# Optimization experiments

Hardware: AMD Instinct MI355X
Metric: run time of the kernel (lower is better)

Reference implementation:

```python
import jax, jax.numpy as jnp
import numpy as np

B, S, D, H = 2, 2048, 512, 8
HD = D // H  # head_size = 64
EPS = 1e-5


def _layer_norm(x, g, b):
    m = jnp.mean(x, axis=-1, keepdims=True)
    v = jnp.mean(jnp.square(x - m), axis=-1, keepdims=True)
    return (x - m) * jax.lax.rsqrt(v + EPS) * g + b


def setup_inputs() -> dict:
    key = jax.random.key(0)
    ks = jax.random.split(key, 16)
    s_in = 1.0 / np.sqrt(D)
    s_ff = 1.0 / np.sqrt(4 * D)
    return {
        "x": jax.random.normal(ks[0], (B, S, D), jnp.float32),
        # per-head q/k/v projections stacked over heads: [H, D, HD]
        "Wq": jax.random.normal(ks[1], (H, D, HD), jnp.float32) * s_in,
        "bq": jax.random.normal(ks[2], (H, HD), jnp.float32) * s_in,
        "Wk": jax.random.normal(ks[3], (H, D, HD), jnp.float32) * s_in,
        "bk": jax.random.normal(ks[4], (H, HD), jnp.float32) * s_in,
        "Wv": jax.random.normal(ks[5], (H, D, HD), jnp.float32) * s_in,
        "bv": jax.random.normal(ks[6], (H, HD), jnp.float32) * s_in,
        "Wp": jax.random.normal(ks[7], (D, D), jnp.float32) * s_in,
        "bp": jax.random.normal(ks[8], (D,), jnp.float32) * s_in,
        "W1": jax.random.normal(ks[9], (D, 4 * D), jnp.float32) * s_in,
        "b1": jax.random.normal(ks[10], (4 * D,), jnp.float32) * s_in,
        "W2": jax.random.normal(ks[11], (4 * D, D), jnp.float32) * s_ff,
        "b2": jax.random.normal(ks[12], (D,), jnp.float32) * s_ff,
        "g1": jnp.ones((D,), jnp.float32),
        "be1": jnp.zeros((D,), jnp.float32),
        "g2": jnp.ones((D,), jnp.float32),
        "be2": jnp.zeros((D,), jnp.float32),
    }


def reference(x, Wq, bq, Wk, bk, Wv, bv, Wp, bp, W1, b1, W2, b2, g1, be1, g2, be2):
    # --- attention sublayer (pre-norm) ---
    xn = _layer_norm(x, g1, be1)                               # [B,S,D]
    q = jnp.einsum('bsd,hde->bhse', xn, Wq) + bq[None, :, None, :]
    k = jnp.einsum('bsd,hde->bhse', xn, Wk) + bk[None, :, None, :]
    v = jnp.einsum('bsd,hde->bhse', xn, Wv) + bv[None, :, None, :]
    # NOTE: original has NO 1/sqrt(head_size) scaling and NO mask
    scores = jnp.einsum('bhse,bhte->bhst', q, k)               # [B,H,S,S]
    w = jax.nn.softmax(scores, axis=-1)
    o = jnp.einsum('bhst,bhte->bhse', w, v)                    # [B,H,S,HD]
    o = o.transpose(0, 2, 1, 3).reshape(x.shape[0], x.shape[1], D)  # concat heads
    attn_out = o @ Wp + bp
    x = x + attn_out
    # --- MLP sublayer (pre-norm) ---
    xn2 = _layer_norm(x, g2, be2)
    h = jax.nn.relu(xn2 @ W1 + b1)
    x = x + (h @ W2 + b2)
    return x
```

## Files before the change

### kernel.cpp

```cpp
#include <hip/hip_runtime.h>
#include <hip/hip_bf16.h>

typedef unsigned short u16;
typedef unsigned long long u64t;
typedef __attribute__((ext_vector_type(8))) short bhalf8;
typedef __attribute__((ext_vector_type(4))) short bhalf4;
typedef __attribute__((ext_vector_type(4))) float f32x4;

#define MFMA16(a, b, c) __builtin_amdgcn_mfma_f32_16x16x32_bf16((a), (b), (c), 0, 0, 0)

#if __has_builtin(__builtin_amdgcn_mfma_f32_16x16x16bf16_1k)
#define HAVE_K16 1
#define MFMAK16(a, b, c) __builtin_amdgcn_mfma_f32_16x16x16bf16_1k((a), (b), (c), 0, 0, 0)
#elif __has_builtin(__builtin_amdgcn_mfma_f32_16x16x16_bf16)
#define HAVE_K16 1
#define MFMAK16(a, b, c) __builtin_amdgcn_mfma_f32_16x16x16_bf16((a), (b), (c), 0, 0, 0)
#else
#define HAVE_K16 0
#endif

#define BB 2
#define SS 2048
#define DD 512
#define HH 8
#define HD 64
#define NT (BB * SS)
#define LOG2E 1.44269504f

#if __has_builtin(__builtin_amdgcn_exp2f)
#define EXP2(x) __builtin_amdgcn_exp2f(x)
#else
#define EXP2(x) exp2f(x)
#endif

__device__ __forceinline__ u16 f2b(float f) {
    unsigned u = __builtin_bit_cast(unsigned, f);
    unsigned r = (u + 0x7fffu + ((u >> 16) & 1u)) >> 16;
    return (u16)r;
}

__device__ __forceinline__ void gl2lds16(const u16* g, u16* l) {
    u16* gn = (u16*)g;
    __builtin_amdgcn_global_load_lds((__attribute__((address_space(1))) void*)gn,
                                     (__attribute__((address_space(3))) void*)l, 16, 0, 0);
}

__global__ __launch_bounds__(256) void k_prep(const float* __restrict__ Wq, const float* __restrict__ Wk,
                                              const float* __restrict__ Wv, const float* __restrict__ Wp,
                                              const float* __restrict__ W1, const float* __restrict__ W2,
                                              const float* __restrict__ bq, const float* __restrict__ bk,
                                              const float* __restrict__ bv,
                                              u16* __restrict__ WqkvT, u16* __restrict__ WpT,
                                              u16* __restrict__ W1T, u16* __restrict__ W2T,
                                              float* __restrict__ biasqkv) {
    int j = blockIdx.x;
    int tx = threadIdx.x, ty = threadIdx.y;
    if (j >= 3072) {
        int i = (j - 3072) * 256 + ty * 32 + tx;
        biasqkv[i] = (i < 512) ? bq[i] : (i < 1024) ? bk[i - 512] : bv[i - 1024];
        return;
    }
    __shared__ float tile[32][33];
    const float* src; u16* dst; int R, C, tr, tc;
    if (j < 768) {
        int m = j >> 8, rem = j & 255, h = rem >> 5, tl = rem & 31;
        tr = tl >> 1; tc = tl & 1;
        src = (m == 0 ? Wq : (m == 1 ? Wk : Wv)) + h * 32768;
        dst = WqkvT + m * 262144 + h * 32768;
        R = 512; C = 64;
    } else if (j < 1024) { int tl = j - 768;  tr = tl >> 4; tc = tl & 15; src = Wp; dst = WpT; R = 512;  C = 512;  }
    else if (j < 2048)   { int tl = j - 1024; tr = tl >> 6; tc = tl & 63; src = W1; dst = W1T; R = 512;  C = 2048; }
    else                 { int tl = j - 2048; tr = tl >> 4; tc = tl & 15; src = W2; dst = W2T; R = 2048; C = 512;  }
    int c = tc * 32 + tx;
#pragma unroll
    for (int i = 0; i < 4; i++)
        tile[ty + i * 8][tx] = src[(size_t)(tr * 32 + ty + i * 8) * C + c];
    __syncthreads();
    int r2 = tr * 32 + tx;
#pragma unroll
    for (int i = 0; i < 4; i++)
        dst[(size_t)(tc * 32 + ty + i * 8) * R + r2] = f2b(tile[tx][ty + i * 8]);
}

__global__ __launch_bounds__(256) void k_layernorm(const float* __restrict__ x,
                                                   const float* __restrict__ g,
                                                   const float* __restrict__ be,
                                                   u16* __restrict__ out) {
    int wave = threadIdx.x >> 6, lane = threadIdx.x & 63;
    int row = blockIdx.x * 4 + wave;
    const float* xr = x + (size_t)row * DD;
    int c = lane * 8;
    float4 v0 = *(const float4*)(xr + c);
    float4 v1 = *(const float4*)(xr + c + 4);
    float s  = v0.x + v0.y + v0.z + v0.w + v1.x + v1.y + v1.z + v1.w;
    float sq = v0.x*v0.x + v0.y*v0.y + v0.z*v0.z + v0.w*v0.w
             + v1.x*v1.x + v1.y*v1.y + v1.z*v1.z + v1.w*v1.w;
#pragma unroll
    for (int m = 1; m < 64; m <<= 1) {
        s  += __shfl_xor(s, m);
        sq += __shfl_xor(sq, m);
    }
    float mean = s * (1.0f / DD);
    float var  = sq * (1.0f / DD) - mean * mean;
    float rstd = rsqrtf(var + 1e-5f);
    float4 g0 = *(const float4*)(g + c);
    float4 g1 = *(const float4*)(g + c + 4);
    float4 b0 = *(const float4*)(be + c);
    float4 b1 = *(const float4*)(be + c + 4);
    float xv[8] = {v0.x, v0.y, v0.z, v0.w, v1.x, v1.y, v1.z, v1.w};
    float gv[8] = {g0.x, g0.y, g0.z, g0.w, g1.x, g1.y, g1.z, g1.w};
    float bv[8] = {b0.x, b0.y, b0.z, b0.w, b1.x, b1.y, b1.z, b1.w};
    union { bhalf8 v; u16 u[8]; } pk;
#pragma unroll
    for (int i = 0; i < 8; i++) pk.u[i] = f2b((xv[i] - mean) * rstd * gv[i] + bv[i]);
    *(bhalf8*)(out + (size_t)row * DD + c) = pk.v;
}

template<int BM, int BN, int WR, int WC, int MI, int NI, int MODE>
__global__ __launch_bounds__(256) void k_gemm(const u16* __restrict__ A, const u16* __restrict__ Bt,
                                              const float* __restrict__ bias,
                                              int lda, int ldb, int kLen, int N,
                                              const float* __restrict__ resid,
                                              float* __restrict__ outF, u16* __restrict__ outB,
                                              u16* __restrict__ qd, u16* __restrict__ kd,
                                              u16* __restrict__ vtd) {
    constexpr int WM = MI * 16;
    constexpr int WN = NI * 16;
    static_assert(WR * WM == BM && WC * WN == BN && WR * WC == 4, "cfg");
    constexpr int ACH = BM / 32;
    constexpr int BCH = BN / 32;
    __shared__ u16 As[BM * 64];
    __shared__ u16 Bs[BN * 64];
    int t = threadIdx.x;
    int wave = t >> 6, lane = t & 63, quad = lane >> 4, l16 = lane & 15;
    int wr, wc;
    if (WC == 1)      { wr = wave; wc = 0; }
    else if (WR == 1) { wr = 0;    wc = wave; }
    else              { wr = wave >> 1; wc = wave & 1; }
    int m0 = blockIdx.y * BM, n0 = blockIdx.x * BN;

    f32x4 acc[MI][NI] = {};

    int srow = lane >> 3;
    int scol = (lane & 7) * 8;
    const u16* Ag = A  + (size_t)(m0 + srow) * lda + scol;
    const u16* Bg = Bt + (size_t)(n0 + srow) * ldb + scol;

    for (int k0 = 0; k0 < kLen; k0 += 64) {
        __syncthreads();
#pragma unroll
        for (int c = 0; c < ACH; c++) {
            int ch = wave * ACH + c;
            gl2lds16(Ag + (size_t)(ch * 8) * lda + k0, &As[ch * 512]);
        }
#pragma unroll
        for (int c = 0; c < BCH; c++) {
            int ch = wave * BCH + c;
            gl2lds16(Bg + (size_t)(ch * 8) * ldb + k0, &Bs[ch * 512]);
        }
        __syncthreads();
#pragma unroll
        for (int h = 0; h < 2; h++) {
            bhalf8 af[MI], bf[NI];
#pragma unroll
            for (int mi = 0; mi < MI; mi++)
                af[mi] = *(bhalf8*)&As[(wr * WM + mi * 16 + l16) * 64 + h * 32 + quad * 8];
#pragma unroll
            for (int ni = 0; ni < NI; ni++)
                bf[ni] = *(bhalf8*)&Bs[(wc * WN + ni * 16 + l16) * 64 + h * 32 + quad * 8];
#pragma unroll
            for (int mi = 0; mi < MI; mi++)
#pragma unroll
                for (int ni = 0; ni < NI; ni++)
                    acc[mi][ni] = MFMA16(af[mi], bf[ni], acc[mi][ni]);
        }
    }

#pragma unroll
    for (int mi = 0; mi < MI; mi++)
#pragma unroll
        for (int ni = 0; ni < NI; ni++) {
            f32x4 a = acc[mi][ni];
            int gc = n0 + wc * WN + ni * 16 + l16;
            int gr0 = m0 + wr * WM + mi * 16 + quad * 4;
            float bsv = bias[gc];
            if (MODE == 0) {
                int mm = gc >> 9, cc = gc & 511;
                int hh = cc >> 6, e = cc & 63;
                int b = gr0 >> 11, s0 = gr0 & 2047;
                if (mm == 2) {
                    u64t pk = 0;
#pragma unroll
                    for (int r = 0; r < 4; r++) pk |= (u64t)f2b(a[r] + bsv) << (16 * r);
                    *(u64t*)&vtd[((size_t)(b * HH + hh) * HD + e) * SS + s0] = pk;
                } else if (mm == 0) {
#pragma unroll
                    for (int r = 0; r < 4; r++)
                        qd[((size_t)(b * HH + hh) * SS + s0 + r) * HD + e] = f2b((a[r] + bsv) * LOG2E);
                } else {
#pragma unroll
                    for (int r = 0; r < 4; r++)
                        kd[((size_t)(b * HH + hh) * SS + s0 + r) * HD + e] = f2b(a[r] + bsv);
                }
            } else if (MODE == 1) {
#pragma unroll
                for (int r = 0; r < 4; r++) {
                    size_t idx = (size_t)(gr0 + r) * N + gc;
                    outF[idx] = a[r] + bsv + resid[idx];
                }
            } else {
#pragma unroll
                for (int r = 0; r < 4; r++)
                    outB[(size_t)(gr0 + r) * N + gc] = f2b(fmaxf(a[r] + bsv, 0.0f));
            }
        }
}

__global__ __launch_bounds__(256) void k_attention(const u16* __restrict__ q,
                                                   const u16* __restrict__ k,
                                                   const u16* __restrict__ vt,
                                                   float* __restrict__ Opart,
                                                   float* __restrict__ lsum) {
    __shared__ u16 Ks[128 * 72];
    __shared__ u16 Vs[64 * 136];
    int bh = blockIdx.x, qt = blockIdx.y, kspl = blockIdx.z;
    int t = threadIdx.x, wave = t >> 6, lane = t & 63, quad = lane >> 4, l16 = lane & 15;
    const u16* qb = q  + (size_t)bh * SS * HD;
    const u16* kb = k  + (size_t)bh * SS * HD;
    const u16* vb = vt + (size_t)bh * HD * SS;

    int srow = qt * 64 + wave * 16 + l16;
    bhalf8 qf0 = *(const bhalf8*)(qb + (size_t)srow * HD + quad * 8);
    bhalf8 qf1 = *(const bhalf8*)(qb + (size_t)srow * HD + 32 + quad * 8);

    f32x4 oacc[4] = {};
    float rsum = 0.f;

    int kr = t >> 1, kc = (t & 1) * 32;
    int vr = t >> 2, vc = (t & 3) * 32;
    const u16* kp = kb + ((size_t)kspl * 1024 + kr) * HD + kc;
    const u16* vp = vb + (size_t)vr * SS + kspl * 1024 + vc;
    u16* ksd = &Ks[kr * 72 + kc];
    u16* vsd = &Vs[vr * 136 + vc];

    bhalf8 kreg[4], vreg[4];
#pragma unroll
    for (int i = 0; i < 4; i++) {
        kreg[i] = *(const bhalf8*)(kp + i * 8);
        vreg[i] = *(const bhalf8*)(vp + i * 8);
    }

    for (int it = 0; it < 8; it++) {
        __syncthreads();
#pragma unroll
        for (int i = 0; i < 4; i++) {
            *(bhalf8*)(ksd + i * 8) = kreg[i];
            *(bhalf8*)(vsd + i * 8) = vreg[i];
        }
        __syncthreads();
        if (it < 7) {
            const u16* kn = kp + (size_t)(it + 1) * 128 * HD;
            const u16* vn = vp + (it + 1) * 128;
#pragma unroll
            for (int i = 0; i < 4; i++) {
                kreg[i] = *(const bhalf8*)(kn + i * 8);
                vreg[i] = *(const bhalf8*)(vn + i * 8);
            }
        }

        f32x4 sacc[8];
#pragma unroll
        for (int nt = 0; nt < 8; nt++) {
            bhalf8 kf0 = *(bhalf8*)&Ks[(nt * 16 + l16) * 72 + quad * 8];
            bhalf8 kf1 = *(bhalf8*)&Ks[(nt * 16 + l16) * 72 + 32 + quad * 8];
            f32x4 s = {};
            s = MFMA16(kf0, qf0, s);
            s = MFMA16(kf1, qf1, s);
            sacc[nt] = s;
        }

#if HAVE_K16
        bhalf4 pa[8];
#pragma unroll
        for (int nt = 0; nt < 8; nt++) {
            union { bhalf4 v; u16 u[4]; } pk;
#pragma unroll
            for (int r = 0; r < 4; r++) {
                float p = EXP2(sacc[nt][r]);
                rsum += p;
                pk.u[r] = f2b(p);
            }
            pa[nt] = pk.v;
        }
#pragma unroll
        for (int nt = 0; nt < 8; nt++)
#pragma unroll
            for (int et = 0; et < 4; et++) {
                bhalf4 vf = *(bhalf4*)&Vs[(et * 16 + l16) * 136 + nt * 16 + quad * 4];
                oacc[et] = MFMAK16(pa[nt], vf, oacc[et]);
            }
#else
        bhalf8 pa[8];
#pragma unroll
        for (int nt = 0; nt < 8; nt++) {
            union { bhalf8 v; u16 u[8]; } pk;
#pragma unroll
            for (int r = 0; r < 4; r++) {
                float p = EXP2(sacc[nt][r]);
                rsum += p;
                pk.u[r] = f2b(p);
            }
#pragma unroll
            for (int r = 4; r < 8; r++) pk.u[r] = 0;
            pa[nt] = pk.v;
        }
#pragma unroll
        for (int nt = 0; nt < 8; nt++)
#pragma unroll
            for (int et = 0; et < 4; et++) {
                union { bhalf8 v; bhalf4 h[2]; } vf;
                vf.h[0] = *(bhalf4*)&Vs[(et * 16 + l16) * 136 + nt * 16 + quad * 4];
                vf.h[1] = (bhalf4){0, 0, 0, 0};
                oacc[et] = MFMA16(pa[nt], vf.v, oacc[et]);
            }
#endif
    }

    rsum += __shfl_xor(rsum, 16);
    rsum += __shfl_xor(rsum, 32);

    int sbase = qt * 64 + wave * 16;
    float* Ob = Opart + ((size_t)(kspl * 16 + bh) * SS + sbase) * HD;
#pragma unroll
    for (int et = 0; et < 4; et++)
#pragma unroll
        for (int r = 0; r < 4; r++)
            Ob[(quad * 4 + r) * HD + et * 16 + l16] = oacc[et][r];
    if (quad == 0)
        lsum[(size_t)(kspl * 16 + bh) * SS + sbase + l16] = rsum;
}

__global__ __launch_bounds__(256) void k_combine(const float* __restrict__ Opart,
                                                 const float* __restrict__ lsum,
                                                 u16* __restrict__ oc) {
    int tid = blockIdx.x * 256 + threadIdx.x;
    int c4 = tid & 15, s = (tid >> 4) & 2047, bh = tid >> 15;
    size_t i0 = ((size_t)bh * SS + s) * HD + c4 * 4;
    float4 p0 = *(const float4*)(Opart + i0);
    float4 p1 = *(const float4*)(Opart + (size_t)16 * SS * HD + i0);
    float l = lsum[(size_t)bh * SS + s] + lsum[(size_t)16 * SS + (size_t)bh * SS + s];
    float inv = 1.0f / l;
    u64t pk = 0;
    pk |= (u64t)f2b((p0.x + p1.x) * inv);
    pk |= (u64t)f2b((p0.y + p1.y) * inv) << 16;
    pk |= (u64t)f2b((p0.z + p1.z) * inv) << 32;
    pk |= (u64t)f2b((p0.w + p1.w) * inv) << 48;
    int b = bh >> 3, h = bh & 7;
    *(u64t*)&oc[((size_t)b * SS + s) * DD + h * HD + c4 * 4] = pk;
}

extern "C" void kernel_launch(void* const* d_in, const int* in_sizes, int n_in,
                              void* d_out, int out_size, void* d_ws, size_t ws_size,
                              hipStream_t stream) {
    const float* x   = (const float*)d_in[0];
    const float* Wq  = (const float*)d_in[1];
    const float* bq  = (const float*)d_in[2];
    const float* Wk  = (const float*)d_in[3];
    const float* bk  = (const float*)d_in[4];
    const float* Wv  = (const float*)d_in[5];
    const float* bv  = (const float*)d_in[6];
    const float* Wp  = (const float*)d_in[7];
    const float* bp  = (const float*)d_in[8];
    const float* W1  = (const float*)d_in[9];
    const float* b1  = (const float*)d_in[10];
    const float* W2  = (const float*)d_in[11];
    const float* b2  = (const float*)d_in[12];
    const float* g1  = (const float*)d_in[13];
    const float* be1 = (const float*)d_in[14];
    const float* g2  = (const float*)d_in[15];
    const float* be2 = (const float*)d_in[16];

    char* ws = (char*)d_ws;
    u16*   WqkvT   = (u16*)(ws + 0);
    u16*   WpT     = (u16*)(ws + 1572864);
    u16*   W1T     = (u16*)(ws + 2097152);
    u16*   W2T     = (u16*)(ws + 4194304);
    float* biasqkv = (float*)(ws + 6291456);
    u16*   xn      = (u16*)(ws + 6297600);
    u16*   qB      = (u16*)(ws + 10491904);
    u16*   kB      = (u16*)(ws + 14686208);
    u16*   vTb     = (u16*)(ws + 18880512);
    u16*   oc      = (u16*)(ws + 23074816);
    float* x1      = (float*)(ws + 27269120);
    u16*   xn2     = (u16*)(ws + 35657728);
    u16*   hbuf    = (u16*)(ws + 39852032);
    float* Opart   = (float*)hbuf;
    float* lsum    = (float*)xn;

    k_prep<<<3078, dim3(32, 8), 0, stream>>>(Wq, Wk, Wv, Wp, W1, W2, bq, bk, bv,
                                             WqkvT, WpT, W1T, W2T, biasqkv);
    k_layernorm<<<NT / 4, 256, 0, stream>>>(x, g1, be1, xn);
    k_gemm<64, 128, 1, 4, 4, 2, 0><<<dim3(12, 64), 256, 0, stream>>>(
        xn, WqkvT, biasqkv, 512, 512, 512, 1536, nullptr, nullptr, nullptr, qB, kB, vTb);
    k_attention<<<dim3(16, 32, 2), 256, 0, stream>>>(qB, kB, vTb, Opart, lsum);
    k_combine<<<2048, 256, 0, stream>>>(Opart, lsum, oc);
    k_gemm<64, 64, 2, 2, 2, 2, 1><<<dim3(8, 64), 256, 0, stream>>>(
        oc, WpT, bp, 512, 512, 512, 512, x, x1, nullptr, nullptr, nullptr, nullptr);
    k_layernorm<<<NT / 4, 256, 0, stream>>>(x1, g2, be2, xn2);
    k_gemm<64, 128, 1, 4, 4, 2, 2><<<dim3(16, 64), 256, 0, stream>>>(
        xn2, W1T, b1, 512, 512, 512, 2048, nullptr, nullptr, hbuf, nullptr, nullptr, nullptr);
    k_gemm<64, 64, 2, 2, 2, 2, 1><<<dim3(8, 64), 256, 0, stream>>>(
        hbuf, W2T, b2, 2048, 2048, 2048, 512, x1, (float*)d_out, nullptr, nullptr, nullptr, nullptr);
}
```

Before: 213.2 us.

## Deepen GEMM K-tile to 128, use fixed 2x2 warp grid, double attention query rows per wave

The GEMM kernel now stages 128-wide K slices in LDS instead of 64, halving the number of barrier-separated load/compute iterations. It also switches to a fixed 2x2 wave layout for all configurations. The attention kernel processes 32 query rows per wave (two 16-row groups), so each K/V tile loaded into LDS is reused across twice as many queries, halving the grid in the query dimension. The softmax/PV stage is fused per key sub-tile to limit register pressure, but extra accumulators and the larger LDS footprint may reduce occupancy.

```diff
diff --git a/kernel.cpp b/kernel.cpp
--- a/kernel.cpp
+++ b/kernel.cpp
@@ -116,7 +116,7 @@
     *(bhalf8*)(out + (size_t)row * DD + c) = pk.v;
 }
 
-template<int BM, int BN, int WR, int WC, int MI, int NI, int MODE>
+template<int BM, int BN, int MI, int NI, int MODE>
 __global__ __launch_bounds__(256) void k_gemm(const u16* __restrict__ A, const u16* __restrict__ Bt,
                                               const float* __restrict__ bias,
                                               int lda, int ldb, int kLen, int N,
@@ -126,48 +126,45 @@
                                               u16* __restrict__ vtd) {
     constexpr int WM = MI * 16;
     constexpr int WN = NI * 16;
-    static_assert(WR * WM == BM && WC * WN == BN && WR * WC == 4, "cfg");
-    constexpr int ACH = BM / 32;
-    constexpr int BCH = BN / 32;
-    __shared__ u16 As[BM * 64];
-    __shared__ u16 Bs[BN * 64];
+    static_assert(2 * WM == BM && 2 * WN == BN, "cfg");
+    constexpr int ACH = BM / 4;
+    constexpr int BCH = BN / 4;
+    __shared__ u16 As[BM * 128];
+    __shared__ u16 Bs[BN * 128];
     int t = threadIdx.x;
     int wave = t >> 6, lane = t & 63, quad = lane >> 4, l16 = lane & 15;
-    int wr, wc;
-    if (WC == 1)      { wr = wave; wc = 0; }
-    else if (WR == 1) { wr = 0;    wc = wave; }
-    else              { wr = wave >> 1; wc = wave & 1; }
+    int wr = wave >> 1, wc = wave & 1;
     int m0 = blockIdx.y * BM, n0 = blockIdx.x * BN;
 
     f32x4 acc[MI][NI] = {};
 
-    int srow = lane >> 3;
-    int scol = (lane & 7) * 8;
+    int srow = lane >> 4;
+    int scol = (lane & 15) * 8;
     const u16* Ag = A  + (size_t)(m0 + srow) * lda + scol;
     const u16* Bg = Bt + (size_t)(n0 + srow) * ldb + scol;
 
-    for (int k0 = 0; k0 < kLen; k0 += 64) {
+    for (int k0 = 0; k0 < kLen; k0 += 128) {
         __syncthreads();
 #pragma unroll
-        for (int c = 0; c < ACH; c++) {
-            int ch = wave * ACH + c;
-            gl2lds16(Ag + (size_t)(ch * 8) * lda + k0, &As[ch * 512]);
-        }
-#pragma unroll
-        for (int c = 0; c < BCH; c++) {
-            int ch = wave * BCH + c;
-            gl2lds16(Bg + (size_t)(ch * 8) * ldb + k0, &Bs[ch * 512]);
+        for (int c = 0; c < ACH / 4; c++) {
+            int ch = wave * (ACH / 4) + c;
+            gl2lds16(Ag + (size_t)(ch * 4) * lda + k0, &As[ch * 512]);
+        }
+#pragma unroll
+        for (int c = 0; c < BCH / 4; c++) {
+            int ch = wave * (BCH / 4) + c;
+            gl2lds16(Bg + (size_t)(ch * 4) * ldb + k0, &Bs[ch * 512]);
         }
         __syncthreads();
 #pragma unroll
-        for (int h = 0; h < 2; h++) {
+        for (int h = 0; h < 4; h++) {
             bhalf8 af[MI], bf[NI];
 #pragma unroll
             for (int mi = 0; mi < MI; mi++)
-                af[mi] = *(bhalf8*)&As[(wr * WM + mi * 16 + l16) * 64 + h * 32 + quad * 8];
+                af[mi] = *(bhalf8*)&As[(wr * WM + mi * 16 + l16) * 128 + h * 32 + quad * 8];
 #pragma unroll
             for (int ni = 0; ni < NI; ni++)
-                bf[ni] = *(bhalf8*)&Bs[(wc * WN + ni * 16 + l16) * 64 + h * 32 + quad * 8];
+                bf[ni] = *(bhalf8*)&Bs[(wc * WN + ni * 16 + l16) * 128 + h * 32 + quad * 8];
 #pragma unroll
             for (int mi = 0; mi < MI; mi++)
 #pragma unroll
@@ -229,12 +226,17 @@
     const u16* kb = k  + (size_t)bh * SS * HD;
     const u16* vb = vt + (size_t)bh * HD * SS;
 
-    int srow = qt * 64 + wave * 16 + l16;
-    bhalf8 qf0 = *(const bhalf8*)(qb + (size_t)srow * HD + quad * 8);
-    bhalf8 qf1 = *(const bhalf8*)(qb + (size_t)srow * HD + 32 + quad * 8);
-
-    f32x4 oacc[4] = {};
-    float rsum = 0.f;
+    bhalf8 qfa0, qfa1, qfb0, qfb1;
+    {
+        int r0 = qt * 128 + wave * 32 + l16;
+        qfa0 = *(const bhalf8*)(qb + (size_t)r0 * HD + quad * 8);
+        qfa1 = *(const bhalf8*)(qb + (size_t)r0 * HD + 32 + quad * 8);
+        qfb0 = *(const bhalf8*)(qb + (size_t)(r0 + 16) * HD + quad * 8);
+        qfb1 = *(const bhalf8*)(qb + (size_t)(r0 + 16) * HD + 32 + quad * 8);
+    }
+
+    f32x4 oacc[2][4] = {};
+    float rsa = 0.f, rsb = 0.f;
 
     int kr = t >> 1, kc = (t & 1) * 32;
     int vr = t >> 2, vc = (t & 3) * 32;
@@ -268,76 +270,68 @@
             }
         }
 
-        f32x4 sacc[8];
 #pragma unroll
         for (int nt = 0; nt < 8; nt++) {
             bhalf8 kf0 = *(bhalf8*)&Ks[(nt * 16 + l16) * 72 + quad * 8];
             bhalf8 kf1 = *(bhalf8*)&Ks[(nt * 16 + l16) * 72 + 32 + quad * 8];
-            f32x4 s = {};
-            s = MFMA16(kf0, qf0, s);
-            s = MFMA16(kf1, qf1, s);
-            sacc[nt] = s;
-        }
-
+            f32x4 sa = {}, sb = {};
+            sa = MFMA16(kf0, qfa0, sa);
+            sa = MFMA16(kf1, qfa1, sa);
+            sb = MFMA16(kf0, qfb0, sb);
+            sb = MFMA16(kf1, qfb1, sb);
 #if HAVE_K16
-        bhalf4 pa[8];
-#pragma unroll
-        for (int nt = 0; nt < 8; nt++) {
-            union { bhalf4 v; u16 u[4]; } pk;
+            union { bhalf4 v; u16 u[4]; } pa, pb;
 #pragma unroll
             for (int r = 0; r < 4; r++) {
-                float p = EXP2(sacc[nt][r]);
-                rsum += p;
-                pk.u[r] = f2b(p);
-            }
-            pa[nt] = pk.v;
-        }
-#pragma unroll
-        for (int nt = 0; nt < 8; nt++)
+                float p0 = EXP2(sa[r]);
+                float p1 = EXP2(sb[r]);
+                rsa += p0; rsb += p1;
+                pa.u[r] = f2b(p0); pb.u[r] = f2b(p1);
+            }
 #pragma unroll
             for (int et = 0; et < 4; et++) {
                 bhalf4 vf = *(bhalf4*)&Vs[(et * 16 + l16) * 136 + nt * 16 + quad * 4];
-                oacc[et] = MFMAK16(pa[nt], vf, oacc[et]);
+                oacc[0][et] = MFMAK16(pa.v, vf, oacc[0][et]);
+                oacc[1][et] = MFMAK16(pb.v, vf, oacc[1][et]);
             }
 #else
-        bhalf8 pa[8];
-#pragma unroll
-        for (int nt = 0; nt < 8; nt++) {
-            union { bhalf8 v; u16 u[8]; } pk;
+            union { bhalf8 v; u16 u[8]; } pa, pb;
 #pragma unroll
             for (int r = 0; r < 4; r++) {
-                float p = EXP2(sacc[nt][r]);
-                rsum += p;
-                pk.u[r] = f2b(p);
-            }
-#pragma unroll
-            for (int r = 4; r < 8; r++) pk.u[r] = 0;
-            pa[nt] = pk.v;
-        }
-#pragma unroll
-        for (int nt = 0; nt < 8; nt++)
+                float p0 = EXP2(sa[r]);
+                float p1 = EXP2(sb[r]);
+                rsa += p0; rsb += p1;
+                pa.u[r] = f2b(p0); pb.u[r] = f2b(p1);
+            }
+#pragma unroll
+            for (int r = 4; r < 8; r++) { pa.u[r] = 0; pb.u[r] = 0; }
 #pragma unroll
             for (int et = 0; et < 4; et++) {
                 union { bhalf8 v; bhalf4 h[2]; } vf;
                 vf.h[0] = *(bhalf4*)&Vs[(et * 16 + l16) * 136 + nt * 16 + quad * 4];
                 vf.h[1] = (bhalf4){0, 0, 0, 0};
-                oacc[et] = MFMA16(pa[nt], vf.v, oacc[et]);
+                oacc[0][et] = MFMA16(pa.v, vf.v, oacc[0][et]);
+                oacc[1][et] = MFMA16(pb.v, vf.v, oacc[1][et]);
             }
 #endif
-    }
-
-    rsum += __shfl_xor(rsum, 16);
-    rsum += __shfl_xor(rsum, 32);
-
-    int sbase = qt * 64 + wave * 16;
-    float* Ob = Opart + ((size_t)(kspl * 16 + bh) * SS + sbase) * HD;
-#pragma unroll
-    for (int et = 0; et < 4; et++)
-#pragma unroll
-        for (int r = 0; r < 4; r++)
-            Ob[(quad * 4 + r) * HD + et * 16 + l16] = oacc[et][r];
-    if (quad == 0)
-        lsum[(size_t)(kspl * 16 + bh) * SS + sbase + l16] = rsum;
+        }
+    }
+
+    rsa += __shfl_xor(rsa, 16); rsa += __shfl_xor(rsa, 32);
+    rsb += __shfl_xor(rsb, 16); rsb += __shfl_xor(rsb, 32);
+
+#pragma unroll
+    for (int qc = 0; qc < 2; qc++) {
+        int sbase = qt * 128 + wave * 32 + qc * 16;
+        float* Ob = Opart + ((size_t)(kspl * 16 + bh) * SS + sbase) * HD;
+#pragma unroll
+        for (int et = 0; et < 4; et++)
+#pragma unroll
+            for (int r = 0; r < 4; r++)
+                Ob[(quad * 4 + r) * HD + et * 16 + l16] = oacc[qc][et][r];
+        if (quad == 0)
+            lsum[(size_t)(kspl * 16 + bh) * SS + sbase + l16] = (qc == 0 ? rsa : rsb);
+    }
 }
 
 __global__ __launch_bounds__(256) void k_combine(const float* __restrict__ Opart,
@@ -400,15 +394,15 @@
     k_prep<<<3078, dim3(32, 8), 0, stream>>>(Wq, Wk, Wv, Wp, W1, W2, bq, bk, bv,
                                              WqkvT, WpT, W1T, W2T, biasqkv);
     k_layernorm<<<NT / 4, 256, 0, stream>>>(x, g1, be1, xn);
-    k_gemm<64, 128, 1, 4, 4, 2, 0><<<dim3(12, 64), 256, 0, stream>>>(
+    k_gemm<64, 128, 2, 4, 0><<<dim3(12, 64), 256, 0, stream>>>(
         xn, WqkvT, biasqkv, 512, 512, 512, 1536, nullptr, nullptr, nullptr, qB, kB, vTb);
-    k_attention<<<dim3(16, 32, 2), 256, 0, stream>>>(qB, kB, vTb, Opart, lsum);
+    k_attention<<<dim3(16, 16, 2), 256, 0, stream>>>(qB, kB, vTb, Opart, lsum);
     k_combine<<<2048, 256, 0, stream>>>(Opart, lsum, oc);
-    k_gemm<64, 64, 2, 2, 2, 2, 1><<<dim3(8, 64), 256, 0, stream>>>(
+    k_gemm<64, 64, 2, 2, 1><<<dim3(8, 64), 256, 0, stream>>>(
         oc, WpT, bp, 512, 512, 512, 512, x, x1, nullptr, nullptr, nullptr, nullptr);
     k_layernorm<<<NT / 4, 256, 0, stream>>>(x1, g2, be2, xn2);
-    k_gemm<64, 128, 1, 4, 4, 2, 2><<<dim3(16, 64), 256, 0, stream>>>(
+    k_gemm<64, 128, 2, 4, 2><<<dim3(16, 64), 256, 0, stream>>>(
         xn2, W1T, b1, 512, 512, 512, 2048, nullptr, nullptr, hbuf, nullptr, nullptr, nullptr);
-    k_gemm<64, 64, 2, 2, 2, 2, 1><<<dim3(8, 64), 256, 0, stream>>>(
+    k_gemm<64, 64, 2, 2, 1><<<dim3(8, 64), 256, 0, stream>>>(
         hbuf, W2T, b2, 2048, 2048, 2048, 512, x1, (float*)d_out, nullptr, nullptr, nullptr, nullptr);
 }
```

Result: slower. 233.4 us (+9.5%).
